# Optimization experiments

Hardware: AMD Instinct MI355X
Metric: run time of the kernel (lower is better)

Reference implementation:

```python
import jax, jax.numpy as jnp
import numpy as np

B, L, V, H = 2, 2048, 1024, 16
HD = V // H  # head size 64
EPS = 1e-3   # keras LayerNormalization default


def setup_inputs() -> dict:
    key = jax.random.key(0)
    ks = jax.random.split(key, 10)
    scale = 1.0 / np.sqrt(V)
    return {
        "query": jax.random.normal(ks[0], (B, L, V), jnp.float32),
        "key_t": jax.random.normal(ks[1], (B, L, V), jnp.float32),
        "value": jax.random.normal(ks[2], (B, L, V), jnp.float32),
        "Wq": jax.random.normal(ks[3], (H, V, HD), jnp.float32) * scale,
        "Wk": jax.random.normal(ks[4], (H, V, HD), jnp.float32) * scale,
        "Wv": jax.random.normal(ks[5], (H, V, HD), jnp.float32) * scale,
        "gamma": jnp.ones((V,), jnp.float32),
        "beta": jnp.zeros((V,), jnp.float32),
        "query_mask": jax.random.randint(ks[6], (B, L), 0, 2, jnp.int32),
        "value_mask": jax.random.randint(ks[7], (B, L), 0, 2, jnp.int32),
    }


def reference(query, key_t, value, Wq, Wk, Wv, gamma, beta, query_mask, value_mask):
    qm = query_mask.astype(jnp.float32)  # (B,L)
    vm = value_mask.astype(jnp.float32)  # (B,L)

    # per-head no-bias Dense projections, batched over heads
    Q = jnp.einsum('blv,hvd->bhld', query, Wq)
    K = jnp.einsum('blv,hvd->bhld', key_t, Wk)
    Vh = jnp.einsum('blv,hvd->bhld', value, Wv)

    scores = jnp.einsum('bhld,bhmd->bhlm', Q, K) / jnp.sqrt(jnp.float32(HD))
    attn = jax.nn.softmax(scores, axis=-1)

    # post-softmax multiplicative masking (faithful to original)
    tri = jnp.tril(jnp.ones((L, L), jnp.float32))  # (L,L) causal
    attn = attn * tri[None, None, :, :]
    attn = attn * qm[:, None, :, None] * vm[:, None, None, :]

    heads = jnp.einsum('bhlm,bhmd->bhld', attn, Vh)
    x = heads.transpose(0, 2, 1, 3).reshape(B, L, V)  # concat heads

    # dropout is identity at inference
    y = x + query
    mu = jnp.mean(y, axis=-1, keepdims=True)
    var = jnp.mean((y - mu) ** 2, axis=-1, keepdims=True)
    return gamma * (y - mu) * jax.lax.rsqrt(var + EPS) + beta
```

## Files before the change

### kernel.cpp

```cpp
#include <hip/hip_runtime.h>
#include <math.h>

constexpr int NB = 2;
constexpr int SL = 2048;
constexpr int NV = 1024;
constexpr int NH = 16;
constexpr int DH = 64;
constexpr float LN_EPS = 1e-3f;

typedef __bf16 bf16_t;
typedef __bf16 v8bf __attribute__((ext_vector_type(8)));
typedef float  v4f  __attribute__((ext_vector_type(4)));

__device__ __forceinline__ unsigned pack_bf16(float a, float b) {
  unsigned short ua = __builtin_bit_cast(unsigned short, (bf16_t)a);
  unsigned short ub = __builtin_bit_cast(unsigned short, (bf16_t)b);
  return (unsigned)ua | ((unsigned)ub << 16);
}
__device__ __forceinline__ void async_cp16(const void* g, void* l) {
  __builtin_amdgcn_global_load_lds(
      (const __attribute__((address_space(1))) unsigned int*)g,
      (__attribute__((address_space(3))) unsigned int*)l, 16, 0, 0);
}
__device__ __forceinline__ void drain_dma() {
  asm volatile("s_waitcnt vmcnt(0)" ::: "memory");
}

__global__ __launch_bounds__(256)
void acvt(const float* __restrict__ q, const float* __restrict__ k,
          const float* __restrict__ v, bf16_t* __restrict__ oq,
          bf16_t* __restrict__ ok, bf16_t* __restrict__ ov) {
  const int z = blockIdx.y;
  const float* src = z == 0 ? q : (z == 1 ? k : v);
  bf16_t*      dst = z == 0 ? oq : (z == 1 ? ok : ov);
  const size_t i = ((size_t)blockIdx.x * 256 + threadIdx.x) * 4;
  float4 f = *(const float4*)(src + i);
  uint2 u = {pack_bf16(f.x, f.y), pack_bf16(f.z, f.w)};
  *(uint2*)(dst + i) = u;
}

__global__ __launch_bounds__(256)
void wcvt(const float* __restrict__ Wq, const float* __restrict__ Wk,
          const float* __restrict__ Wv, bf16_t* __restrict__ Wt) {
  __shared__ float ls[64][65];
  const int z = blockIdx.z;
  const float* W = z == 0 ? Wq : (z == 1 ? Wk : Wv);
  const float sc = z == 0 ? 0.125f * 1.44269504f : 1.0f;
  const int h = blockIdx.y, v0 = blockIdx.x * 64;
  const int t = threadIdx.x;
  const int rr = t >> 4, c4 = t & 15;
  const float* src = W + ((size_t)h * NV + v0) * DH;
#pragma unroll
  for (int it = 0; it < 4; ++it) {
    float4 f = *(const float4*)(src + (size_t)(rr + it * 16) * DH + c4 * 4);
    ls[rr + it * 16][c4 * 4 + 0] = f.x;
    ls[rr + it * 16][c4 * 4 + 1] = f.y;
    ls[rr + it * 16][c4 * 4 + 2] = f.z;
    ls[rr + it * 16][c4 * 4 + 3] = f.w;
  }
  __syncthreads();
  const int dd = t >> 2, vq = t & 3;
  bf16_t tmp[16];
#pragma unroll
  for (int i = 0; i < 16; ++i) tmp[i] = (bf16_t)(ls[vq * 16 + i][dd] * sc);
  bf16_t* dst = Wt + ((size_t)z * NV + h * 64 + dd) * NV + v0 + vq * 16;
  *(v8bf*)dst = *(v8bf*)&tmp[0];
  *(v8bf*)(dst + 8) = *(v8bf*)&tmp[8];
}

__global__ __launch_bounds__(256, 4)
void proj_mfma(const bf16_t* __restrict__ A0, const bf16_t* __restrict__ A1,
               const bf16_t* __restrict__ A2, const bf16_t* __restrict__ Wtb,
               const int* __restrict__ vmask,
               bf16_t* __restrict__ O0, bf16_t* __restrict__ O1,
               bf16_t* __restrict__ O2) {
  __shared__ __align__(16) bf16_t Asb[2][128 * 32];
  __shared__ __align__(16) bf16_t Wsb[2][128 * 32];

  const int z = blockIdx.z;
  const bf16_t* A   = z == 0 ? A0 : (z == 1 ? A1 : A2);
  bf16_t*       out = z == 0 ? O0 : (z == 1 ? O1 : O2);
  const bf16_t* W   = Wtb + (size_t)z * NV * NV;

  const int t = threadIdx.x, w = t >> 6, lane = t & 63;
  const int g = lane >> 4, lx = lane & 15;
  const int m0 = blockIdx.x * 128, n0 = blockIdx.y * 128;
  const int rbase = (w >> 1) * 64, cbase = (w & 1) * 64;

  const int sr = lane >> 2;
  const int sc = (lane & 3);
  auto stageA = [&](int k0, int buf) {
#pragma unroll
    for (int s = 0; s < 2; ++s) {
      const int r = w * 32 + s * 16 + sr;
      const int c = sc ^ (r & 3);
      async_cp16(A + (size_t)(m0 + r) * NV + k0 + c * 8,
                 (char*)Asb[buf] + (w * 32 + s * 16) * 64);
    }
  };
  auto stageW = [&](int k0, int buf) {
#pragma unroll
    for (int s = 0; s < 2; ++s) {
      const int r = w * 32 + s * 16 + sr;
      const int c = sc ^ (r & 3);
      async_cp16(W + (size_t)(n0 + r) * NV + k0 + c * 8,
                 (char*)Wsb[buf] + (w * 32 + s * 16) * 64);
    }
  };

  v4f acc[4][4] = {};
  stageA(0, 0);
  stageW(0, 0);

  for (int it = 0; it < 32; ++it) {
    const int buf = it & 1;
    drain_dma();
    __syncthreads();
    if (it < 31) {
      stageA((it + 1) * 32, buf ^ 1);
      stageW((it + 1) * 32, buf ^ 1);
    }
    v8bf af[4], wf[4];
#pragma unroll
    for (int rt = 0; rt < 4; ++rt) {
      const int row = rbase + rt * 16 + lx;
      af[rt] = *(const v8bf*)((const char*)Asb[buf] + row * 64 +
                              ((g ^ (row & 3)) * 16));
    }
#pragma unroll
    for (int ct = 0; ct < 4; ++ct) {
      const int row = cbase + ct * 16 + lx;
      wf[ct] = *(const v8bf*)((const char*)Wsb[buf] + row * 64 +
                              ((g ^ (row & 3)) * 16));
    }
#pragma unroll
    for (int rt = 0; rt < 4; ++rt)
#pragma unroll
      for (int ct = 0; ct < 4; ++ct)
        acc[rt][ct] = __builtin_amdgcn_mfma_f32_16x16x32_bf16(
            af[rt], wf[ct], acc[rt][ct], 0, 0, 0);
  }

  if (z < 2) {
#pragma unroll
    for (int rt = 0; rt < 4; ++rt) {
#pragma unroll
      for (int reg = 0; reg < 4; ++reg) {
        const int row = m0 + rbase + rt * 16 + g * 4 + reg;
        const int b = row >> 11, l = row & (SL - 1);
#pragma unroll
        for (int ct = 0; ct < 4; ++ct) {
          const int n = n0 + cbase + ct * 16 + lx;
          const int h = n >> 6, d = n & 63;
          out[((size_t)(b * NH + h) * SL + l) * DH + d] = (bf16_t)acc[rt][ct][reg];
        }
      }
    }
  } else {
#pragma unroll
    for (int rt = 0; rt < 4; ++rt) {
      const int row = m0 + rbase + rt * 16 + g * 4;
      const int b = row >> 11, l = row & (SL - 1);
      float vm0 = (float)vmask[b * SL + l + 0];
      float vm1 = (float)vmask[b * SL + l + 1];
      float vm2 = (float)vmask[b * SL + l + 2];
      float vm3 = (float)vmask[b * SL + l + 3];
#pragma unroll
      for (int ct = 0; ct < 4; ++ct) {
        const int n = n0 + cbase + ct * 16 + lx;
        const int h = n >> 6, d = n & 63;
        uint2 u = {pack_bf16(acc[rt][ct][0] * vm0, acc[rt][ct][1] * vm1),
                   pack_bf16(acc[rt][ct][2] * vm2, acc[rt][ct][3] * vm3)};
        *(uint2*)&out[((size_t)(b * NH + h) * DH + d) * SL + l] = u;
      }
    }
  }
}

__global__ __launch_bounds__(256, 3)
void attn_mfma(const bf16_t* __restrict__ Qg, const bf16_t* __restrict__ Kg,
               const bf16_t* __restrict__ Vtg_all, const int* __restrict__ qmask,
               float* __restrict__ Xout) {
  __shared__ __align__(16) bf16_t kbuf[2][64 * 64];
  __shared__ __align__(16) bf16_t vbuf[2][64 * 64];
  __shared__ __align__(16) bf16_t Ps[4][32][72];

  const int id = blockIdx.x;
  const int bh = (id & 7) | ((id >> 7) << 3);
  const int qraw = (id >> 3) & 15;
  const int qb = ((id >> 8) & 1) ? qraw : 15 - qraw;
  const int t = threadIdx.x, w = t >> 6, lane = t & 63;
  const int g = lane >> 4, lx = lane & 15;
  const int b = bh >> 4, h = bh & 15;
  const int l0 = qb * 128;
  const int lastAct = 2 * qb + 1;

  const bf16_t* Kb  = Kg + (size_t)bh * SL * DH;
  const bf16_t* Vtg = Vtg_all + (size_t)bh * DH * SL;

  v8bf qf[2][2];
#pragma unroll
  for (int qt = 0; qt < 2; ++qt)
#pragma unroll
    for (int ks = 0; ks < 2; ++ks)
      qf[qt][ks] = *(const v8bf*)&Qg[((size_t)bh * SL + l0 + w * 32 + qt * 16 + lx) * DH +
                                     ks * 32 + g * 8];

  v4f O[2][4] = {};
  float suml[2] = {0.f, 0.f};

  const int sr_off = lane >> 3, sc_l = lane & 7;
  auto stageK = [&](int mb, int buf) {
#pragma unroll
    for (int s = 0; s < 2; ++s) {
      const int r = w * 16 + s * 8 + sr_off;
      const int c = sc_l ^ (r & 7);
      async_cp16(Kb + (size_t)(mb + r) * DH + c * 8,
                 (char*)kbuf[buf] + (w * 16 + s * 8) * 128);
    }
  };
  auto stageV = [&](int mb, int buf) {
#pragma unroll
    for (int s = 0; s < 2; ++s) {
      const int r = w * 16 + s * 8 + sr_off;
      const int c = sc_l ^ (r & 7);
      async_cp16(Vtg + (size_t)r * SL + mb + c * 8,
                 (char*)vbuf[buf] + (w * 16 + s * 8) * 128);
    }
  };

  stageK(0, 0);
  stageV(0, 0);

  for (int mt = 0; mt <= lastAct; ++mt) {
    const int pb = mt & 1;
    drain_dma();
    __syncthreads();
    if (mt < SL / 64 - 1)  stageK((mt + 1) * 64, pb ^ 1);
    if (mt + 1 <= lastAct) stageV((mt + 1) * 64, pb ^ 1);

    v4f S[4][2];
#pragma unroll
    for (int mt2 = 0; mt2 < 4; ++mt2) {
      S[mt2][0] = (v4f){0.f, 0.f, 0.f, 0.f};
      S[mt2][1] = (v4f){0.f, 0.f, 0.f, 0.f};
    }
#pragma unroll
    for (int ks = 0; ks < 2; ++ks)
#pragma unroll
      for (int mt2 = 0; mt2 < 4; ++mt2) {
        const int row = mt2 * 16 + lx;
        v8bf kf = *(const v8bf*)((const char*)kbuf[pb] + row * 128 +
                                 (((ks * 4 + g) ^ (lx & 7)) * 16));
#pragma unroll
        for (int qt = 0; qt < 2; ++qt)
          S[mt2][qt] = __builtin_amdgcn_mfma_f32_16x16x32_bf16(
              kf, qf[qt][ks], S[mt2][qt], 0, 0, 0);
      }

    const bool diagzone = (mt >= 2 * qb);
#pragma unroll
    for (int mt2 = 0; mt2 < 4; ++mt2)
#pragma unroll
      for (int qt = 0; qt < 2; ++qt) {
        float e0 = __builtin_amdgcn_exp2f(S[mt2][qt][0]);
        float e1 = __builtin_amdgcn_exp2f(S[mt2][qt][1]);
        float e2 = __builtin_amdgcn_exp2f(S[mt2][qt][2]);
        float e3 = __builtin_amdgcn_exp2f(S[mt2][qt][3]);
        suml[qt] += (e0 + e1) + (e2 + e3);
        if (diagzone) {
          const int ml = mt * 64 + mt2 * 16 + g * 4;
          const int ql = l0 + w * 32 + qt * 16 + lx;
          e0 = (ml + 0 <= ql) ? e0 : 0.f;
          e1 = (ml + 1 <= ql) ? e1 : 0.f;
          e2 = (ml + 2 <= ql) ? e2 : 0.f;
          e3 = (ml + 3 <= ql) ? e3 : 0.f;
        }
        uint2 u = {pack_bf16(e0, e1), pack_bf16(e2, e3)};
        *(uint2*)&Ps[w][qt * 16 + lx][mt2 * 16 + g * 4] = u;
      }

    __builtin_amdgcn_wave_barrier();

#pragma unroll
    for (int ks = 0; ks < 2; ++ks) {
      v8bf pf[2];
#pragma unroll
      for (int qt = 0; qt < 2; ++qt)
        pf[qt] = *(const v8bf*)&Ps[w][qt * 16 + lx][ks * 32 + g * 8];
#pragma unroll
      for (int dt = 0; dt < 4; ++dt) {
        const int row = dt * 16 + lx;
        v8bf vf = *(const v8bf*)((const char*)vbuf[pb] + row * 128 +
                                 (((ks * 4 + g) ^ (lx & 7)) * 16));
#pragma unroll
        for (int qt = 0; qt < 2; ++qt)
          O[qt][dt] = __builtin_amdgcn_mfma_f32_16x16x32_bf16(
              pf[qt], vf, O[qt][dt], 0, 0, 0);
      }
    }
  }

  for (int mt = lastAct + 1; mt < SL / 64; ++mt) {
    const int pb = mt & 1;
    drain_dma();
    __syncthreads();
    if (mt < SL / 64 - 1) stageK((mt + 1) * 64, pb ^ 1);
    v4f S[4][2];
#pragma unroll
    for (int mt2 = 0; mt2 < 4; ++mt2) {
      S[mt2][0] = (v4f){0.f, 0.f, 0.f, 0.f};
      S[mt2][1] = (v4f){0.f, 0.f, 0.f, 0.f};
    }
#pragma unroll
    for (int ks = 0; ks < 2; ++ks)
#pragma unroll
      for (int mt2 = 0; mt2 < 4; ++mt2) {
        const int row = mt2 * 16 + lx;
        v8bf kf = *(const v8bf*)((const char*)kbuf[pb] + row * 128 +
                                 (((ks * 4 + g) ^ (lx & 7)) * 16));
#pragma unroll
        for (int qt = 0; qt < 2; ++qt)
          S[mt2][qt] = __builtin_amdgcn_mfma_f32_16x16x32_bf16(
              kf, qf[qt][ks], S[mt2][qt], 0, 0, 0);
      }
#pragma unroll
    for (int mt2 = 0; mt2 < 4; ++mt2)
#pragma unroll
      for (int qt = 0; qt < 2; ++qt)
        suml[qt] += (__builtin_amdgcn_exp2f(S[mt2][qt][0]) +
                     __builtin_amdgcn_exp2f(S[mt2][qt][1])) +
                    (__builtin_amdgcn_exp2f(S[mt2][qt][2]) +
                     __builtin_amdgcn_exp2f(S[mt2][qt][3]));
  }

  suml[0] += __shfl_xor(suml[0], 16); suml[0] += __shfl_xor(suml[0], 32);
  suml[1] += __shfl_xor(suml[1], 16); suml[1] += __shfl_xor(suml[1], 32);
#pragma unroll
  for (int qt = 0; qt < 2; ++qt) {
#pragma unroll
    for (int reg = 0; reg < 4; ++reg) {
      const int q = l0 + w * 32 + qt * 16 + g * 4 + reg;
      const float den = __shfl(suml[qt], g * 4 + reg);
      const float inv = (float)qmask[b * SL + q] / den;
#pragma unroll
      for (int dt = 0; dt < 4; ++dt)
        Xout[((size_t)(b * SL + q)) * NV + h * DH + dt * 16 + lx] =
            O[qt][dt][reg] * inv;
    }
  }
}

__global__ __launch_bounds__(256)
void ln_kernel(const float* __restrict__ X, const float* __restrict__ query,
               const float* __restrict__ gamma, const float* __restrict__ beta,
               float* __restrict__ out) {
  const int row = blockIdx.x * 4 + (threadIdx.x >> 6);
  const int lane = threadIdx.x & 63;
  const float* xr = X + (size_t)row * NV;
  const float* qr = query + (size_t)row * NV;
  float4 y[4];
  float s = 0.f, ss = 0.f;
#pragma unroll
  for (int i = 0; i < 4; ++i) {
    const int col = lane * 4 + i * 256;
    float4 xv = *(const float4*)(xr + col);
    float4 qv = *(const float4*)(qr + col);
    y[i].x = xv.x + qv.x; y[i].y = xv.y + qv.y;
    y[i].z = xv.z + qv.z; y[i].w = xv.w + qv.w;
    s  += (y[i].x + y[i].y) + (y[i].z + y[i].w);
    ss += (y[i].x * y[i].x + y[i].y * y[i].y) +
          (y[i].z * y[i].z + y[i].w * y[i].w);
  }
#pragma unroll
  for (int off = 1; off < 64; off <<= 1) {
    s  += __shfl_xor(s, off);
    ss += __shfl_xor(ss, off);
  }
  const float mu   = s * (1.f / NV);
  const float var  = ss * (1.f / NV) - mu * mu;
  const float rstd = rsqrtf(var + LN_EPS);
#pragma unroll
  for (int i = 0; i < 4; ++i) {
    const int col = lane * 4 + i * 256;
    float4 gv = *(const float4*)(gamma + col);
    float4 bv = *(const float4*)(beta + col);
    float4 o;
    o.x = gv.x * (y[i].x - mu) * rstd + bv.x;
    o.y = gv.y * (y[i].y - mu) * rstd + bv.y;
    o.z = gv.z * (y[i].z - mu) * rstd + bv.z;
    o.w = gv.w * (y[i].w - mu) * rstd + bv.w;
    *(float4*)(out + (size_t)row * NV + col) = o;
  }
}

extern "C" void kernel_launch(void* const* d_in, const int* in_sizes, int n_in,
                              void* d_out, int out_size, void* d_ws, size_t ws_size,
                              hipStream_t stream) {
  const float* query = (const float*)d_in[0];
  const float* key_t = (const float*)d_in[1];
  const float* value = (const float*)d_in[2];
  const float* Wq    = (const float*)d_in[3];
  const float* Wk    = (const float*)d_in[4];
  const float* Wv    = (const float*)d_in[5];
  const float* gamma = (const float*)d_in[6];
  const float* beta  = (const float*)d_in[7];
  const int*   qmask = (const int*)d_in[8];
  const int*   vmask = (const int*)d_in[9];
  float* out = (float*)d_out;

  const size_t per = (size_t)NB * NH * SL * DH;
  bf16_t* Qws = (bf16_t*)d_ws;
  bf16_t* Kws = Qws + per;
  bf16_t* Vws = Kws + per;
  bf16_t* Wtb = Vws + per;
  bf16_t* Aq  = Wtb + (size_t)3 * NV * NV;
  bf16_t* Ak  = Aq + per;
  bf16_t* Av  = Ak + per;

  acvt<<<dim3((NB * SL * NV) / (256 * 4), 3), 256, 0, stream>>>(
      query, key_t, value, Aq, Ak, Av);
  wcvt<<<dim3(16, 16, 3), 256, 0, stream>>>(Wq, Wk, Wv, Wtb);
  proj_mfma<<<dim3(32, 8, 3), 256, 0, stream>>>(Aq, Ak, Av, Wtb,
                                                vmask, Qws, Kws, Vws);
  attn_mfma<<<512, 256, 0, stream>>>(Qws, Kws, Vws, qmask, out);
  ln_kernel<<<NB * SL / 4, 256, 0, stream>>>(out, query, gamma, beta, out);
}
```

Measured before the change: 206.3 us.

## Halve attention query tile to 64 rows and swizzle P staging buffer

Each attention block now handles 64 query rows, 16 per wave instead of 32, so the grid doubles to 1024 blocks and the occupancy hint rises from 3 to 4 blocks per CU. The aim is finer causal load balancing and more resident waves to hide latency. The P scratch tile moves to a compact XOR-swizzled layout to avoid LDS bank conflicts. In exchange, every block still streams the full K sequence for the softmax denominator, so K traffic doubles and each LDS K/V fragment now feeds only one MFMA instead of two.

```diff
diff --git a/kernel.cpp b/kernel.cpp
--- a/kernel.cpp
+++ b/kernel.cpp
@@ -177,37 +177,35 @@
   }
 }
 
-__global__ __launch_bounds__(256, 3)
+__global__ __launch_bounds__(256, 4)
 void attn_mfma(const bf16_t* __restrict__ Qg, const bf16_t* __restrict__ Kg,
                const bf16_t* __restrict__ Vtg_all, const int* __restrict__ qmask,
                float* __restrict__ Xout) {
   __shared__ __align__(16) bf16_t kbuf[2][64 * 64];
   __shared__ __align__(16) bf16_t vbuf[2][64 * 64];
-  __shared__ __align__(16) bf16_t Ps[4][32][72];
+  __shared__ __align__(16) bf16_t Ps[4][16 * 64];
 
   const int id = blockIdx.x;
-  const int bh = (id & 7) | ((id >> 7) << 3);
-  const int qraw = (id >> 3) & 15;
-  const int qb = ((id >> 8) & 1) ? qraw : 15 - qraw;
+  const int bh = (id & 7) | ((id >> 8) << 3);
+  const int qraw = (id >> 3) & 31;
+  const int qb = ((id >> 8) & 1) ? qraw : 31 - qraw;
   const int t = threadIdx.x, w = t >> 6, lane = t & 63;
   const int g = lane >> 4, lx = lane & 15;
   const int b = bh >> 4, h = bh & 15;
-  const int l0 = qb * 128;
-  const int lastAct = 2 * qb + 1;
+  const int l0 = qb * 64;
+  const int lastAct = qb;
 
   const bf16_t* Kb  = Kg + (size_t)bh * SL * DH;
   const bf16_t* Vtg = Vtg_all + (size_t)bh * DH * SL;
 
-  v8bf qf[2][2];
-#pragma unroll
-  for (int qt = 0; qt < 2; ++qt)
-#pragma unroll
-    for (int ks = 0; ks < 2; ++ks)
-      qf[qt][ks] = *(const v8bf*)&Qg[((size_t)bh * SL + l0 + w * 32 + qt * 16 + lx) * DH +
-                                     ks * 32 + g * 8];
-
-  v4f O[2][4] = {};
-  float suml[2] = {0.f, 0.f};
+  v8bf qf[2];
+#pragma unroll
+  for (int ks = 0; ks < 2; ++ks)
+    qf[ks] = *(const v8bf*)&Qg[((size_t)bh * SL + l0 + w * 16 + lx) * DH +
+                               ks * 32 + g * 8];
+
+  v4f O[4] = {};
+  float suml = 0.f;
 
   const int sr_off = lane >> 3, sc_l = lane & 7;
   auto stageK = [&](int mb, int buf) {
@@ -239,12 +237,9 @@
     if (mt < SL / 64 - 1)  stageK((mt + 1) * 64, pb ^ 1);
     if (mt + 1 <= lastAct) stageV((mt + 1) * 64, pb ^ 1);
 
-    v4f S[4][2];
-#pragma unroll
-    for (int mt2 = 0; mt2 < 4; ++mt2) {
-      S[mt2][0] = (v4f){0.f, 0.f, 0.f, 0.f};
-      S[mt2][1] = (v4f){0.f, 0.f, 0.f, 0.f};
-    }
+    v4f S[4];
+#pragma unroll
+    for (int mt2 = 0; mt2 < 4; ++mt2) S[mt2] = (v4f){0.f, 0.f, 0.f, 0.f};
 #pragma unroll
     for (int ks = 0; ks < 2; ++ks)
 #pragma unroll
@@ -252,51 +247,44 @@
         const int row = mt2 * 16 + lx;
         v8bf kf = *(const v8bf*)((const char*)kbuf[pb] + row * 128 +
                                  (((ks * 4 + g) ^ (lx & 7)) * 16));
-#pragma unroll
-        for (int qt = 0; qt < 2; ++qt)
-          S[mt2][qt] = __builtin_amdgcn_mfma_f32_16x16x32_bf16(
-              kf, qf[qt][ks], S[mt2][qt], 0, 0, 0);
-      }
-
-    const bool diagzone = (mt >= 2 * qb);
-#pragma unroll
-    for (int mt2 = 0; mt2 < 4; ++mt2)
-#pragma unroll
-      for (int qt = 0; qt < 2; ++qt) {
-        float e0 = __builtin_amdgcn_exp2f(S[mt2][qt][0]);
-        float e1 = __builtin_amdgcn_exp2f(S[mt2][qt][1]);
-        float e2 = __builtin_amdgcn_exp2f(S[mt2][qt][2]);
-        float e3 = __builtin_amdgcn_exp2f(S[mt2][qt][3]);
-        suml[qt] += (e0 + e1) + (e2 + e3);
-        if (diagzone) {
-          const int ml = mt * 64 + mt2 * 16 + g * 4;
-          const int ql = l0 + w * 32 + qt * 16 + lx;
-          e0 = (ml + 0 <= ql) ? e0 : 0.f;
-          e1 = (ml + 1 <= ql) ? e1 : 0.f;
-          e2 = (ml + 2 <= ql) ? e2 : 0.f;
-          e3 = (ml + 3 <= ql) ? e3 : 0.f;
-        }
-        uint2 u = {pack_bf16(e0, e1), pack_bf16(e2, e3)};
-        *(uint2*)&Ps[w][qt * 16 + lx][mt2 * 16 + g * 4] = u;
-      }
+        S[mt2] = __builtin_amdgcn_mfma_f32_16x16x32_bf16(kf, qf[ks], S[mt2],
+                                                         0, 0, 0);
+      }
+
+    const bool diagzone = (mt == qb);
+#pragma unroll
+    for (int mt2 = 0; mt2 < 4; ++mt2) {
+      float e0 = __builtin_amdgcn_exp2f(S[mt2][0]);
+      float e1 = __builtin_amdgcn_exp2f(S[mt2][1]);
+      float e2 = __builtin_amdgcn_exp2f(S[mt2][2]);
+      float e3 = __builtin_amdgcn_exp2f(S[mt2][3]);
+      suml += (e0 + e1) + (e2 + e3);
+      if (diagzone) {
+        const int ml = mt * 64 + mt2 * 16 + g * 4;
+        const int ql = l0 + w * 16 + lx;
+        e0 = (ml + 0 <= ql) ? e0 : 0.f;
+        e1 = (ml + 1 <= ql) ? e1 : 0.f;
+        e2 = (ml + 2 <= ql) ? e2 : 0.f;
+        e3 = (ml + 3 <= ql) ? e3 : 0.f;
+      }
+      uint2 u = {pack_bf16(e0, e1), pack_bf16(e2, e3)};
+      *(uint2*)((char*)Ps[w] + lx * 128 +
+                ((mt2 * 32 + g * 8) ^ ((lx & 7) << 4))) = u;
+    }
 
     __builtin_amdgcn_wave_barrier();
 
 #pragma unroll
     for (int ks = 0; ks < 2; ++ks) {
-      v8bf pf[2];
-#pragma unroll
-      for (int qt = 0; qt < 2; ++qt)
-        pf[qt] = *(const v8bf*)&Ps[w][qt * 16 + lx][ks * 32 + g * 8];
+      v8bf pf = *(const v8bf*)((const char*)Ps[w] + lx * 128 +
+                               ((ks * 64 + g * 16) ^ ((lx & 7) << 4)));
 #pragma unroll
       for (int dt = 0; dt < 4; ++dt) {
         const int row = dt * 16 + lx;
         v8bf vf = *(const v8bf*)((const char*)vbuf[pb] + row * 128 +
                                  (((ks * 4 + g) ^ (lx & 7)) * 16));
-#pragma unroll
-        for (int qt = 0; qt < 2; ++qt)
-          O[qt][dt] = __builtin_amdgcn_mfma_f32_16x16x32_bf16(
-              pf[qt], vf, O[qt][dt], 0, 0, 0);
+        O[dt] = __builtin_amdgcn_mfma_f32_16x16x32_bf16(pf, vf, O[dt],
+                                                        0, 0, 0);
       }
     }
   }
@@ -306,12 +294,9 @@
     drain_dma();
     __syncthreads();
     if (mt < SL / 64 - 1) stageK((mt + 1) * 64, pb ^ 1);
-    v4f S[4][2];
-#pragma unroll
-    for (int mt2 = 0; mt2 < 4; ++mt2) {
-      S[mt2][0] = (v4f){0.f, 0.f, 0.f, 0.f};
-      S[mt2][1] = (v4f){0.f, 0.f, 0.f, 0.f};
-    }
+    v4f S[4];
+#pragma unroll
+    for (int mt2 = 0; mt2 < 4; ++mt2) S[mt2] = (v4f){0.f, 0.f, 0.f, 0.f};
 #pragma unroll
     for (int ks = 0; ks < 2; ++ks)
 #pragma unroll
@@ -319,35 +304,28 @@
         const int row = mt2 * 16 + lx;
         v8bf kf = *(const v8bf*)((const char*)kbuf[pb] + row * 128 +
                                  (((ks * 4 + g) ^ (lx & 7)) * 16));
-#pragma unroll
-        for (int qt = 0; qt < 2; ++qt)
-          S[mt2][qt] = __builtin_amdgcn_mfma_f32_16x16x32_bf16(
-              kf, qf[qt][ks], S[mt2][qt], 0, 0, 0);
+        S[mt2] = __builtin_amdgcn_mfma_f32_16x16x32_bf16(kf, qf[ks], S[mt2],
+                                                         0, 0, 0);
       }
 #pragma unroll
     for (int mt2 = 0; mt2 < 4; ++mt2)
-#pragma unroll
-      for (int qt = 0; qt < 2; ++qt)
-        suml[qt] += (__builtin_amdgcn_exp2f(S[mt2][qt][0]) +
-                     __builtin_amdgcn_exp2f(S[mt2][qt][1])) +
-                    (__builtin_amdgcn_exp2f(S[mt2][qt][2]) +
-                     __builtin_amdgcn_exp2f(S[mt2][qt][3]));
-  }
-
-  suml[0] += __shfl_xor(suml[0], 16); suml[0] += __shfl_xor(suml[0], 32);
-  suml[1] += __shfl_xor(suml[1], 16); suml[1] += __shfl_xor(suml[1], 32);
-#pragma unroll
-  for (int qt = 0; qt < 2; ++qt) {
-#pragma unroll
-    for (int reg = 0; reg < 4; ++reg) {
-      const int q = l0 + w * 32 + qt * 16 + g * 4 + reg;
-      const float den = __shfl(suml[qt], g * 4 + reg);
-      const float inv = (float)qmask[b * SL + q] / den;
-#pragma unroll
-      for (int dt = 0; dt < 4; ++dt)
-        Xout[((size_t)(b * SL + q)) * NV + h * DH + dt * 16 + lx] =
-            O[qt][dt][reg] * inv;
-    }
+      suml += (__builtin_amdgcn_exp2f(S[mt2][0]) +
+               __builtin_amdgcn_exp2f(S[mt2][1])) +
+              (__builtin_amdgcn_exp2f(S[mt2][2]) +
+               __builtin_amdgcn_exp2f(S[mt2][3]));
+  }
+
+  suml += __shfl_xor(suml, 16);
+  suml += __shfl_xor(suml, 32);
+#pragma unroll
+  for (int reg = 0; reg < 4; ++reg) {
+    const int q = l0 + w * 16 + g * 4 + reg;
+    const float den = __shfl(suml, g * 4 + reg);
+    const float inv = (float)qmask[b * SL + q] / den;
+#pragma unroll
+    for (int dt = 0; dt < 4; ++dt)
+      Xout[((size_t)(b * SL + q)) * NV + h * DH + dt * 16 + lx] =
+          O[dt][reg] * inv;
   }
 }
 
@@ -423,6 +401,6 @@
   wcvt<<<dim3(16, 16, 3), 256, 0, stream>>>(Wq, Wk, Wv, Wtb);
   proj_mfma<<<dim3(32, 8, 3), 256, 0, stream>>>(Aq, Ak, Av, Wtb,
                                                 vmask, Qws, Kws, Vws);
-  attn_mfma<<<512, 256, 0, stream>>>(Qws, Kws, Vws, qmask, out);
+  attn_mfma<<<1024, 256, 0, stream>>>(Qws, Kws, Vws, qmask, out);
   ln_kernel<<<NB * SL / 4, 256, 0, stream>>>(out, query, gamma, beta, out);
 }
```

After: 205.6 us. About the same (-0.3%).

## Split attention key tile across wave pairs with 64-row query blocks

Applied to the files above, without the earlier changes.

Query blocks shrink from 128 to 64 rows and the grid doubles to 1024 blocks. Within a block, the four waves are arranged as two query halves by two key halves. Each wave computes partial scores, row sums and outputs over 32 keys, and the partials are combined through shared memory at the end. The intent is more blocks and higher occupancy (launch bounds raised to 4) for better load balance across the causal triangle. The cost is that every K/V tile is now staged twice as often per query row, plus an extra cross-wave reduction and two block syncs.

```diff
diff --git a/kernel.cpp b/kernel.cpp
--- a/kernel.cpp
+++ b/kernel.cpp
@@ -177,23 +177,24 @@
   }
 }
 
-__global__ __launch_bounds__(256, 3)
+__global__ __launch_bounds__(256, 4)
 void attn_mfma(const bf16_t* __restrict__ Qg, const bf16_t* __restrict__ Kg,
                const bf16_t* __restrict__ Vtg_all, const int* __restrict__ qmask,
                float* __restrict__ Xout) {
   __shared__ __align__(16) bf16_t kbuf[2][64 * 64];
   __shared__ __align__(16) bf16_t vbuf[2][64 * 64];
-  __shared__ __align__(16) bf16_t Ps[4][32][72];
+  __shared__ __align__(16) bf16_t Ps[4][32 * 32];
 
   const int id = blockIdx.x;
-  const int bh = (id & 7) | ((id >> 7) << 3);
-  const int qraw = (id >> 3) & 15;
-  const int qb = ((id >> 8) & 1) ? qraw : 15 - qraw;
+  const int bh = (id & 7) | ((id >> 8) << 3);
+  const int qraw = (id >> 3) & 31;
+  const int qb = ((id >> 8) & 1) ? qraw : 31 - qraw;
   const int t = threadIdx.x, w = t >> 6, lane = t & 63;
+  const int wq = w & 1, wm = w >> 1;
   const int g = lane >> 4, lx = lane & 15;
   const int b = bh >> 4, h = bh & 15;
-  const int l0 = qb * 128;
-  const int lastAct = 2 * qb + 1;
+  const int l0 = qb * 64;
+  const int lastAct = qb;
 
   const bf16_t* Kb  = Kg + (size_t)bh * SL * DH;
   const bf16_t* Vtg = Vtg_all + (size_t)bh * DH * SL;
@@ -203,7 +204,7 @@
   for (int qt = 0; qt < 2; ++qt)
 #pragma unroll
     for (int ks = 0; ks < 2; ++ks)
-      qf[qt][ks] = *(const v8bf*)&Qg[((size_t)bh * SL + l0 + w * 32 + qt * 16 + lx) * DH +
+      qf[qt][ks] = *(const v8bf*)&Qg[((size_t)bh * SL + l0 + wq * 32 + qt * 16 + lx) * DH +
                                      ks * 32 + g * 8];
 
   v4f O[2][4] = {};
@@ -239,17 +240,17 @@
     if (mt < SL / 64 - 1)  stageK((mt + 1) * 64, pb ^ 1);
     if (mt + 1 <= lastAct) stageV((mt + 1) * 64, pb ^ 1);
 
-    v4f S[4][2];
-#pragma unroll
-    for (int mt2 = 0; mt2 < 4; ++mt2) {
+    v4f S[2][2];
+#pragma unroll
+    for (int mt2 = 0; mt2 < 2; ++mt2) {
       S[mt2][0] = (v4f){0.f, 0.f, 0.f, 0.f};
       S[mt2][1] = (v4f){0.f, 0.f, 0.f, 0.f};
     }
 #pragma unroll
     for (int ks = 0; ks < 2; ++ks)
 #pragma unroll
-      for (int mt2 = 0; mt2 < 4; ++mt2) {
-        const int row = mt2 * 16 + lx;
+      for (int mt2 = 0; mt2 < 2; ++mt2) {
+        const int row = wm * 32 + mt2 * 16 + lx;
         v8bf kf = *(const v8bf*)((const char*)kbuf[pb] + row * 128 +
                                  (((ks * 4 + g) ^ (lx & 7)) * 16));
 #pragma unroll
@@ -258,9 +259,9 @@
               kf, qf[qt][ks], S[mt2][qt], 0, 0, 0);
       }
 
-    const bool diagzone = (mt >= 2 * qb);
-#pragma unroll
-    for (int mt2 = 0; mt2 < 4; ++mt2)
+    const bool diagzone = (mt == qb);
+#pragma unroll
+    for (int mt2 = 0; mt2 < 2; ++mt2)
 #pragma unroll
       for (int qt = 0; qt < 2; ++qt) {
         float e0 = __builtin_amdgcn_exp2f(S[mt2][qt][0]);
@@ -269,35 +270,34 @@
         float e3 = __builtin_amdgcn_exp2f(S[mt2][qt][3]);
         suml[qt] += (e0 + e1) + (e2 + e3);
         if (diagzone) {
-          const int ml = mt * 64 + mt2 * 16 + g * 4;
-          const int ql = l0 + w * 32 + qt * 16 + lx;
+          const int ml = mt * 64 + wm * 32 + mt2 * 16 + g * 4;
+          const int ql = l0 + wq * 32 + qt * 16 + lx;
           e0 = (ml + 0 <= ql) ? e0 : 0.f;
           e1 = (ml + 1 <= ql) ? e1 : 0.f;
           e2 = (ml + 2 <= ql) ? e2 : 0.f;
           e3 = (ml + 3 <= ql) ? e3 : 0.f;
         }
         uint2 u = {pack_bf16(e0, e1), pack_bf16(e2, e3)};
-        *(uint2*)&Ps[w][qt * 16 + lx][mt2 * 16 + g * 4] = u;
+        *(uint2*)((char*)Ps[w] + (qt * 16 + lx) * 64 +
+                  (((mt2 * 2 + (g >> 1)) ^ (lx & 3)) * 16) + (g & 1) * 8) = u;
       }
 
     __builtin_amdgcn_wave_barrier();
 
-#pragma unroll
-    for (int ks = 0; ks < 2; ++ks) {
-      v8bf pf[2];
+    v8bf pf[2];
+#pragma unroll
+    for (int qt = 0; qt < 2; ++qt)
+      pf[qt] = *(const v8bf*)((const char*)Ps[w] + (qt * 16 + lx) * 64 +
+                              ((g ^ (lx & 3)) * 16));
+#pragma unroll
+    for (int dt = 0; dt < 4; ++dt) {
+      const int row = dt * 16 + lx;
+      v8bf vf = *(const v8bf*)((const char*)vbuf[pb] + row * 128 +
+                               (((wm * 4 + g) ^ (lx & 7)) * 16));
 #pragma unroll
       for (int qt = 0; qt < 2; ++qt)
-        pf[qt] = *(const v8bf*)&Ps[w][qt * 16 + lx][ks * 32 + g * 8];
-#pragma unroll
-      for (int dt = 0; dt < 4; ++dt) {
-        const int row = dt * 16 + lx;
-        v8bf vf = *(const v8bf*)((const char*)vbuf[pb] + row * 128 +
-                                 (((ks * 4 + g) ^ (lx & 7)) * 16));
-#pragma unroll
-        for (int qt = 0; qt < 2; ++qt)
-          O[qt][dt] = __builtin_amdgcn_mfma_f32_16x16x32_bf16(
-              pf[qt], vf, O[qt][dt], 0, 0, 0);
-      }
+        O[qt][dt] = __builtin_amdgcn_mfma_f32_16x16x32_bf16(
+            pf[qt], vf, O[qt][dt], 0, 0, 0);
     }
   }
 
@@ -306,17 +306,17 @@
     drain_dma();
     __syncthreads();
     if (mt < SL / 64 - 1) stageK((mt + 1) * 64, pb ^ 1);
-    v4f S[4][2];
-#pragma unroll
-    for (int mt2 = 0; mt2 < 4; ++mt2) {
+    v4f S[2][2];
+#pragma unroll
+    for (int mt2 = 0; mt2 < 2; ++mt2) {
       S[mt2][0] = (v4f){0.f, 0.f, 0.f, 0.f};
       S[mt2][1] = (v4f){0.f, 0.f, 0.f, 0.f};
     }
 #pragma unroll
     for (int ks = 0; ks < 2; ++ks)
 #pragma unroll
-      for (int mt2 = 0; mt2 < 4; ++mt2) {
-        const int row = mt2 * 16 + lx;
+      for (int mt2 = 0; mt2 < 2; ++mt2) {
+        const int row = wm * 32 + mt2 * 16 + lx;
         v8bf kf = *(const v8bf*)((const char*)kbuf[pb] + row * 128 +
                                  (((ks * 4 + g) ^ (lx & 7)) * 16));
 #pragma unroll
@@ -325,7 +325,7 @@
               kf, qf[qt][ks], S[mt2][qt], 0, 0, 0);
       }
 #pragma unroll
-    for (int mt2 = 0; mt2 < 4; ++mt2)
+    for (int mt2 = 0; mt2 < 2; ++mt2)
 #pragma unroll
       for (int qt = 0; qt < 2; ++qt)
         suml[qt] += (__builtin_amdgcn_exp2f(S[mt2][qt][0]) +
@@ -336,17 +336,43 @@
 
   suml[0] += __shfl_xor(suml[0], 16); suml[0] += __shfl_xor(suml[0], 32);
   suml[1] += __shfl_xor(suml[1], 16); suml[1] += __shfl_xor(suml[1], 32);
-#pragma unroll
-  for (int qt = 0; qt < 2; ++qt) {
-#pragma unroll
-    for (int reg = 0; reg < 4; ++reg) {
-      const int q = l0 + w * 32 + qt * 16 + g * 4 + reg;
-      const float den = __shfl(suml[qt], g * 4 + reg);
-      const float inv = (float)qmask[b * SL + q] / den;
+
+  __syncthreads();
+  float* obuf = (float*)&kbuf[0][0];
+  float* sbuf = (float*)&vbuf[0][0];
+  if (g == 0) {
+    sbuf[((wq * 2 + wm) * 2 + 0) * 16 + lx] = suml[0];
+    sbuf[((wq * 2 + wm) * 2 + 1) * 16 + lx] = suml[1];
+  }
+  if (wm == 1) {
+#pragma unroll
+    for (int qt = 0; qt < 2; ++qt)
 #pragma unroll
       for (int dt = 0; dt < 4; ++dt)
-        Xout[((size_t)(b * SL + q)) * NV + h * DH + dt * 16 + lx] =
-            O[qt][dt][reg] * inv;
+#pragma unroll
+        for (int reg = 0; reg < 4; ++reg)
+          obuf[wq * 2048 + (qt * 16 + g * 4 + reg) * 64 + dt * 16 + lx] =
+              O[qt][dt][reg];
+  }
+  __syncthreads();
+  if (wm == 0) {
+#pragma unroll
+    for (int qt = 0; qt < 2; ++qt) {
+      const float stot = suml[qt] + sbuf[((wq * 2 + 1) * 2 + qt) * 16 + lx];
+#pragma unroll
+      for (int reg = 0; reg < 4; ++reg) {
+        const int q = l0 + wq * 32 + qt * 16 + g * 4 + reg;
+        const float den = __shfl(stot, g * 4 + reg);
+        const float inv = (float)qmask[b * SL + q] / den;
+#pragma unroll
+        for (int dt = 0; dt < 4; ++dt) {
+          const float val =
+              (O[qt][dt][reg] +
+               obuf[wq * 2048 + (qt * 16 + g * 4 + reg) * 64 + dt * 16 + lx]) *
+              inv;
+          Xout[((size_t)(b * SL + q)) * NV + h * DH + dt * 16 + lx] = val;
+        }
+      }
     }
   }
 }
@@ -423,6 +449,6 @@
   wcvt<<<dim3(16, 16, 3), 256, 0, stream>>>(Wq, Wk, Wv, Wtb);
   proj_mfma<<<dim3(32, 8, 3), 256, 0, stream>>>(Aq, Ak, Av, Wtb,
                                                 vmask, Qws, Kws, Vws);
-  attn_mfma<<<512, 256, 0, stream>>>(Qws, Kws, Vws, qmask, out);
+  attn_mfma<<<1024, 256, 0, stream>>>(Qws, Kws, Vws, qmask, out);
   ln_kernel<<<NB * SL / 4, 256, 0, stream>>>(out, query, gamma, beta, out);
 }
```

After: 207.2 us. About the same (+0.5%).
